# Optimization experiments

Hardware: AMD Instinct MI355X
Metric: run time of the kernel (lower is better)

Reference implementation:

```python
import jax, jax.numpy as jnp
import numpy as np

D_MODEL = 4096
N_TYPES = 6  # fixed event_types list in the module


def setup_inputs() -> dict:
    key = jax.random.key(0)
    ks = jax.random.split(key, 7)
    E, B, d = 131072, 16384, D_MODEL
    return {
        "event_type": jax.random.randint(ks[0], (E,), 0, N_TYPES),
        "confidence": jax.random.uniform(ks[1], (E,), jnp.float32),
        "location": jax.random.uniform(ks[2], (E, 2), jnp.float32) * jnp.array([640.0, 480.0], jnp.float32),
        "batch_idx": jax.random.randint(ks[3], (E,), 0, B),
        "batch_size": B,
        "type_emb": jax.random.normal(ks[4], (N_TYPES, d // 4), jnp.float32),
        "W1": jax.random.normal(ks[5], (d // 2, d // 4 + 3), jnp.float32) / np.sqrt(d // 4 + 3).astype(np.float32),
        "b1": jnp.zeros((d // 2,), jnp.float32),
        "W2": jax.random.normal(ks[6], (d, d // 2), jnp.float32) / np.sqrt(d // 2).astype(np.float32),
        "b2": jnp.zeros((d,), jnp.float32),
    }


def reference(event_type, confidence, location, batch_idx, batch_size, type_emb, W1, b1, W2, b2):
    E = confidence.shape[0]
    B = batch_size
    # per-batch-slot max confidence (empty slots -> -inf)
    seg_max = jax.ops.segment_max(confidence, batch_idx, num_segments=B)
    is_top = confidence == seg_max[batch_idx]
    # first event attaining the max (matches torch's max-over-list semantics)
    cand = jnp.where(is_top, jnp.arange(E), E)
    top_idx = jnp.full((B,), E, dtype=cand.dtype).at[batch_idx].min(cand)
    has_event = top_idx < E
    safe_idx = jnp.where(has_event, top_idx, 0)

    emb = type_emb[event_type[safe_idx]]                 # [B, d/4]
    c = confidence[safe_idx][:, None]                    # [B, 1]
    loc = location[safe_idx] / jnp.array([640.0, 480.0], jnp.float32)  # [B, 2]
    feats = jnp.concatenate([emb, c, loc], axis=-1)      # [B, d/4 + 3]

    h = jax.nn.relu(feats @ W1.T + b1)                   # [B, d/2]
    out = h @ W2.T + b2                                  # [B, d]
    return jnp.where(has_event[:, None], out, jnp.zeros((), out.dtype))
```

## Files before the change

### kernel.cpp

```cpp
#include <hip/hip_runtime.h>
#include <hip/hip_bf16.h>

#define NT 6
#define BM 256
#define BN 256
#define BK 32
#define SLOT 16384

typedef __attribute__((ext_vector_type(4))) float f32x4;
typedef __attribute__((ext_vector_type(8))) short bf16x8;

__device__ __forceinline__ short f2bf(float f) {
    __hip_bfloat16 h = __float2bfloat16(f);
    return (short)__builtin_bit_cast(unsigned short, h);
}

__global__ void k_segmax(const float* __restrict__ conf,
                         const int* __restrict__ bidx,
                         unsigned long long* __restrict__ packed, int E) {
    int i = blockIdx.x * blockDim.x + threadIdx.x;
    if (i >= E) return;
    unsigned cb = __float_as_uint(conf[i]);
    unsigned long long p = ((unsigned long long)cb << 32) | (unsigned)(~(unsigned)i);
    atomicMax(&packed[bidx[i]], p);
}

__global__ void k_base(const float* __restrict__ emb, const float* __restrict__ W1,
                       const float* __restrict__ b1, float* __restrict__ base,
                       float* __restrict__ vecs, int d2, int d4) {
    int gw = (blockIdx.x * blockDim.x + threadIdx.x) >> 6;
    int lane = threadIdx.x & 63;
    int t = gw / d2, n = gw % d2;
    const float* e = emb + (size_t)t * d4;
    const float* w = W1 + (size_t)n * (d4 + 3);
    float s = 0.f;
    for (int k = lane; k < d4; k += 64) s += e[k] * w[k];
#pragma unroll
    for (int m = 32; m; m >>= 1) s += __shfl_xor(s, m);
    if (lane == 0) {
        base[gw] = s + b1[n];
        if (t == 0) {
            vecs[n]          = w[d4];
            vecs[d2 + n]     = w[d4 + 1];
            vecs[2 * d2 + n] = w[d4 + 2];
        }
    }
}

__global__ void k_w2cast(const float* __restrict__ W2, short* __restrict__ W2b, long n) {
    long i = ((long)blockIdx.x * blockDim.x + threadIdx.x) * 8;
    if (i >= n) return;
    bf16x8 v;
#pragma unroll
    for (int j = 0; j < 8; ++j) v[j] = f2bf(W2[i + j]);
    *(bf16x8*)(W2b + i) = v;
}

__global__ void k_h(const unsigned long long* __restrict__ packed,
                    const int* __restrict__ etype, const float* __restrict__ loc,
                    const float* __restrict__ base, const float* __restrict__ vecs,
                    float* __restrict__ mask, short* __restrict__ h, int d2) {
    int b = blockIdx.x;
    int tid = threadIdx.x;
    unsigned long long p = packed[b];
    bool has = (p != 0ULL);
    float conf = 0.f, lx = 0.f, ly = 0.f;
    int t = 0;
    if (has) {
        unsigned idx = ~(unsigned)(p & 0xFFFFFFFFu);
        conf = __uint_as_float((unsigned)(p >> 32));
        t  = etype[idx];
        lx = loc[2 * (size_t)idx]     * (1.0f / 640.0f);
        ly = loc[2 * (size_t)idx + 1] * (1.0f / 480.0f);
    }
    if (tid == 0) mask[b] = has ? 1.0f : 0.0f;
    const float* bs = base + (size_t)t * d2;
    const float* cv = vecs;
    const float* xv = vecs + d2;
    const float* yv = vecs + 2 * d2;
    int n0 = tid * 8;
    bf16x8 v;
#pragma unroll
    for (int j = 0; j < 8; ++j) {
        int n = n0 + j;
        float g = bs[n] + conf * cv[n] + lx * xv[n] + ly * yv[n];
        g = fmaxf(g, 0.f);
        v[j] = has ? f2bf(g) : (short)0;
    }
    *(bf16x8*)(h + (size_t)b * d2 + n0) = v;
}


#define GLL(src, dst) __builtin_amdgcn_global_load_lds(                      \
    (const __attribute__((address_space(1))) void*)(src),                    \
    (__attribute__((address_space(3))) void*)(dst), 16, 0, 0)

#define STAGE4(slotp) do {                                                   \
    GLL(pa0, (slotp) + dA0); GLL(pa1, (slotp) + dA1);                        \
    GLL(pb0, (slotp) + dB0); GLL(pb1, (slotp) + dB1);                        \
    pa0 += BK; pa1 += BK; pb0 += BK; pb1 += BK; } while (0)

#define SB __builtin_amdgcn_sched_barrier(0)

__global__ __launch_bounds__(512, 2)
void k_gemm(const short* __restrict__ A, const short* __restrict__ Bm,
            const float* __restrict__ b2, const float* __restrict__ mask,
            float* __restrict__ C, int M, int N, int K, int nbn) {
    __shared__ __align__(16) short lds[4 * SLOT];

    int tid = threadIdx.x;
    int lane = tid & 63;
    int wave = tid >> 6;
    int wr = wave >> 2, wc = wave & 3;

    int bid = blockIdx.x;
    int wg = (bid & 7) * ((int)gridDim.x >> 3) + (bid >> 3);
    int bm = wg / nbn, bn = wg % nbn;
    int row0 = bm * BM, col0 = bn * BN;

    int srow = tid >> 2;
    int chunkL = (tid & 3) ^ ((srow >> 1) & 3);
    const short* pa0 = A + (size_t)(row0 + srow) * K + chunkL * 8;
    const short* pa1 = pa0 + (size_t)128 * K;
    const short* pb0 = Bm + (size_t)(col0 + srow) * K + chunkL * 8;
    const short* pb1 = pb0 + (size_t)128 * K;
    int dA0 = tid * 8, dA1 = 4096 + tid * 8;
    int dB0 = 8192 + tid * 8, dB1 = 12288 + tid * 8;

    int frow = lane & 15, fk = lane >> 4;
    int cp = fk ^ ((frow >> 1) & 3);
    int aoff = (wr * 128 + frow) * 32 + cp * 8;
    int boff = 8192 + (wc * 64 + frow) * 32 + cp * 8;

    f32x4 acc[8][4] = {};

    int KT = K / BK;

    STAGE4(lds + 0 * SLOT);
    STAGE4(lds + 1 * SLOT);
    STAGE4(lds + 2 * SLOT);
    asm volatile("s_waitcnt vmcnt(8)" ::: "memory");
    __builtin_amdgcn_s_barrier();

#pragma unroll 1
    for (int t = 0; t < KT; ++t) {
        const short* sr = lds + (t & 3) * SLOT;
        bf16x8 afA[4], afB[4], bv[4];
#pragma unroll
        for (int n = 0; n < 4; ++n)
            bv[n] = *(const bf16x8*)(sr + boff + n * 512);
#pragma unroll
        for (int m = 0; m < 4; ++m)
            afA[m] = *(const bf16x8*)(sr + aoff + m * 512);
        SB;
#pragma unroll
        for (int m = 0; m < 4; ++m)
            afB[m] = *(const bf16x8*)(sr + aoff + 2048 + m * 512);
        if (t < KT - 3) {
            short* sw = lds + ((t + 3) & 3) * SLOT;
            STAGE4(sw);
        }
        SB;
        asm volatile("s_waitcnt lgkmcnt(4)" ::: "memory");
        SB;
        __builtin_amdgcn_s_setprio(1);
#pragma unroll
        for (int m = 0; m < 4; ++m)
#pragma unroll
            for (int n = 0; n < 4; ++n)
                acc[m][n] = __builtin_amdgcn_mfma_f32_16x16x32_bf16(
                    afA[m], bv[n], acc[m][n], 0, 0, 0);
        SB;
        asm volatile("s_waitcnt lgkmcnt(0)" ::: "memory");
        SB;
#pragma unroll
        for (int m = 0; m < 4; ++m)
#pragma unroll
            for (int n = 0; n < 4; ++n)
                acc[4 + m][n] = __builtin_amdgcn_mfma_f32_16x16x32_bf16(
                    afB[m], bv[n], acc[4 + m][n], 0, 0, 0);
        __builtin_amdgcn_s_setprio(0);
        if (t < KT - 1) {
            if (t < KT - 3)       asm volatile("s_waitcnt vmcnt(8)" ::: "memory");
            else if (t == KT - 3) asm volatile("s_waitcnt vmcnt(4)" ::: "memory");
            else                  asm volatile("s_waitcnt vmcnt(0)" ::: "memory");
            __builtin_amdgcn_s_barrier();
        }
    }

#pragma unroll
    for (int m = 0; m < 8; ++m) {
        int rbase = row0 + wr * 128 + m * 16 + (lane >> 4) * 4;
#pragma unroll
        for (int j = 0; j < 4; ++j) {
            int r = rbase + j;
            float mk = mask[r];
#pragma unroll
            for (int n = 0; n < 4; ++n) {
                int c = col0 + wc * 64 + n * 16 + frow;
                C[(size_t)r * N + c] = (acc[m][n][j] + b2[c]) * mk;
            }
        }
    }
}

extern "C" void kernel_launch(void* const* d_in, const int* in_sizes, int n_in,
                              void* d_out, int out_size, void* d_ws, size_t ws_size,
                              hipStream_t stream) {
    const int* etype   = (const int*)d_in[0];
    const float* conf  = (const float*)d_in[1];
    const float* loc   = (const float*)d_in[2];
    const int* bidx    = (const int*)d_in[3];
    const float* emb   = (const float*)d_in[5];
    const float* W1    = (const float*)d_in[6];
    const float* b1    = (const float*)d_in[7];
    const float* W2    = (const float*)d_in[8];
    const float* b2    = (const float*)d_in[9];
    float* out = (float*)d_out;

    int E  = in_sizes[0];
    int d2 = in_sizes[7];
    int d  = in_sizes[9];
    int d4 = in_sizes[5] / NT;
    int B  = out_size / d;

    char* ws = (char*)d_ws;
    unsigned long long* packed = (unsigned long long*)ws;
    float* mask = (float*)(ws + (size_t)B * 8);
    float* base = mask + B;
    float* vecs = base + NT * d2;
    short* w2b  = (short*)(vecs + 3 * d2);
    short* h    = w2b + (size_t)d * d2;

    hipMemsetAsync(packed, 0, (size_t)B * 8, stream);
    k_segmax<<<(E + 255) / 256, 256, 0, stream>>>(conf, bidx, packed, E);
    k_base<<<(NT * d2) / 4, 256, 0, stream>>>(emb, W1, b1, base, vecs, d2, d4);
    long nw2 = (long)d * d2;
    k_w2cast<<<(int)(nw2 / 8 / 256), 256, 0, stream>>>(W2, w2b, nw2);
    k_h<<<B, 256, 0, stream>>>(packed, etype, loc, base, vecs, mask, h, d2);
    int nbm = B / BM, nbn = d / BN;
    k_gemm<<<dim3(nbm * nbn), dim3(512), 0, stream>>>(h, w2b, b2, mask, out, B, d, d2, nbn);
}
```

Measured before the change: 312.0 us.

## Software-pipeline LDS fragment loads across K iterations with ping-pong B registers

Restructures the GEMM main loop so the next tile's A(0-3) and B fragments are read from LDS while the second half of the current tile's MFMAs is still issuing, using two B register sets that alternate on a 2x unrolled loop. It also splits the global-to-LDS prefetch so A loads and B loads go out at different points in the iteration, and adds an extra barrier so the slot about to be overwritten has been fully read. The goal is to hide LDS read latency behind MFMA work and smooth out memory traffic. The cost is higher register pressure under the 2-wave occupancy bound, and the loop now assumes KT is even.

```diff
diff --git a/kernel.cpp b/kernel.cpp
--- a/kernel.cpp
+++ b/kernel.cpp
@@ -95,12 +95,46 @@
     (const __attribute__((address_space(1))) void*)(src),                    \
     (__attribute__((address_space(3))) void*)(dst), 16, 0, 0)
 
-#define STAGE4(slotp) do {                                                   \
-    GLL(pa0, (slotp) + dA0); GLL(pa1, (slotp) + dA1);                        \
-    GLL(pb0, (slotp) + dB0); GLL(pb1, (slotp) + dB1);                        \
-    pa0 += BK; pa1 += BK; pb0 += BK; pb1 += BK; } while (0)
-
 #define SB __builtin_amdgcn_sched_barrier(0)
+
+#define BODY(T, CBV, NBV)                                                     \
+  {                                                                           \
+    const short* sr_ = lds + ((T) & 3) * SLOT;                                \
+    short* sw_ = lds + (((T) + 3) & 3) * SLOT;                                \
+    \
+    _Pragma("unroll") for (int m = 0; m < 4; ++m)                             \
+        a47[m] = *(const bf16x8*)(sr_ + aoff + 2048 + m * 512);               \
+    __builtin_amdgcn_s_barrier();                                             \
+    SB;                                                                       \
+    if ((T) < KT - 3) { GLL(pa0, sw_ + dA0); GLL(pa1, sw_ + dA1); }           \
+    __builtin_amdgcn_s_setprio(1);                                            \
+    _Pragma("unroll") for (int m = 0; m < 4; ++m)                             \
+      _Pragma("unroll") for (int n = 0; n < 4; ++n)                           \
+        acc[m][n] = __builtin_amdgcn_mfma_f32_16x16x32_bf16(                  \
+            a03[m], CBV[n], acc[m][n], 0, 0, 0);                              \
+    __builtin_amdgcn_s_setprio(0);                                            \
+                                                                     \
+    if ((T) < KT - 3) { GLL(pb0, sw_ + dB0); GLL(pb1, sw_ + dB1);             \
+                        pa0 += BK; pa1 += BK; pb0 += BK; pb1 += BK; }         \
+    if ((T) < KT - 3)       asm volatile("s_waitcnt vmcnt(8)" ::: "memory");  \
+    else if ((T) == KT - 3) asm volatile("s_waitcnt vmcnt(4)" ::: "memory");  \
+    else if ((T) == KT - 2) asm volatile("s_waitcnt vmcnt(0)" ::: "memory");  \
+    __builtin_amdgcn_s_barrier();                                             \
+    SB;                                                                       \
+    if ((T) < KT - 1) {         \
+      const short* sn_ = lds + (((T) + 1) & 3) * SLOT;                        \
+      _Pragma("unroll") for (int n = 0; n < 4; ++n)                           \
+          NBV[n] = *(const bf16x8*)(sn_ + boff + n * 512);                    \
+      _Pragma("unroll") for (int m = 0; m < 4; ++m)                           \
+          a03[m] = *(const bf16x8*)(sn_ + aoff + m * 512);                    \
+    }                                                                         \
+    __builtin_amdgcn_s_setprio(1);                                            \
+    _Pragma("unroll") for (int m = 0; m < 4; ++m)                             \
+      _Pragma("unroll") for (int n = 0; n < 4; ++n)                           \
+        acc[4 + m][n] = __builtin_amdgcn_mfma_f32_16x16x32_bf16(              \
+            a47[m], CBV[n], acc[4 + m][n], 0, 0, 0);                          \
+    __builtin_amdgcn_s_setprio(0);                                            \
+  }
 
 __global__ __launch_bounds__(512, 2)
 void k_gemm(const short* __restrict__ A, const short* __restrict__ Bm,
@@ -133,59 +167,36 @@
     int boff = 8192 + (wc * 64 + frow) * 32 + cp * 8;
 
     f32x4 acc[8][4] = {};
+    bf16x8 a03[4], a47[4], bv0[4], bv1[4];
 
     int KT = K / BK;
 
-    STAGE4(lds + 0 * SLOT);
-    STAGE4(lds + 1 * SLOT);
-    STAGE4(lds + 2 * SLOT);
+    {
+        short* s0 = lds + 0 * SLOT;
+        GLL(pa0, s0 + dA0); GLL(pa1, s0 + dA1); GLL(pb0, s0 + dB0); GLL(pb1, s0 + dB1);
+        pa0 += BK; pa1 += BK; pb0 += BK; pb1 += BK;
+        short* s1 = lds + 1 * SLOT;
+        GLL(pa0, s1 + dA0); GLL(pa1, s1 + dA1); GLL(pb0, s1 + dB0); GLL(pb1, s1 + dB1);
+        pa0 += BK; pa1 += BK; pb0 += BK; pb1 += BK;
+        short* s2 = lds + 2 * SLOT;
+        GLL(pa0, s2 + dA0); GLL(pa1, s2 + dA1); GLL(pb0, s2 + dB0); GLL(pb1, s2 + dB1);
+        pa0 += BK; pa1 += BK; pb0 += BK; pb1 += BK;
+    }
     asm volatile("s_waitcnt vmcnt(8)" ::: "memory");
     __builtin_amdgcn_s_barrier();
+    SB;
+    {
+        const short* s0 = lds + 0 * SLOT;
+#pragma unroll
+        for (int n = 0; n < 4; ++n) bv0[n] = *(const bf16x8*)(s0 + boff + n * 512);
+#pragma unroll
+        for (int m = 0; m < 4; ++m) a03[m] = *(const bf16x8*)(s0 + aoff + m * 512);
+    }
 
 #pragma unroll 1
-    for (int t = 0; t < KT; ++t) {
-        const short* sr = lds + (t & 3) * SLOT;
-        bf16x8 afA[4], afB[4], bv[4];
-#pragma unroll
-        for (int n = 0; n < 4; ++n)
-            bv[n] = *(const bf16x8*)(sr + boff + n * 512);
-#pragma unroll
-        for (int m = 0; m < 4; ++m)
-            afA[m] = *(const bf16x8*)(sr + aoff + m * 512);
-        SB;
-#pragma unroll
-        for (int m = 0; m < 4; ++m)
-            afB[m] = *(const bf16x8*)(sr + aoff + 2048 + m * 512);
-        if (t < KT - 3) {
-            short* sw = lds + ((t + 3) & 3) * SLOT;
-            STAGE4(sw);
-        }
-        SB;
-        asm volatile("s_waitcnt lgkmcnt(4)" ::: "memory");
-        SB;
-        __builtin_amdgcn_s_setprio(1);
-#pragma unroll
-        for (int m = 0; m < 4; ++m)
-#pragma unroll
-            for (int n = 0; n < 4; ++n)
-                acc[m][n] = __builtin_amdgcn_mfma_f32_16x16x32_bf16(
-                    afA[m], bv[n], acc[m][n], 0, 0, 0);
-        SB;
-        asm volatile("s_waitcnt lgkmcnt(0)" ::: "memory");
-        SB;
-#pragma unroll
-        for (int m = 0; m < 4; ++m)
-#pragma unroll
-            for (int n = 0; n < 4; ++n)
-                acc[4 + m][n] = __builtin_amdgcn_mfma_f32_16x16x32_bf16(
-                    afB[m], bv[n], acc[4 + m][n], 0, 0, 0);
-        __builtin_amdgcn_s_setprio(0);
-        if (t < KT - 1) {
-            if (t < KT - 3)       asm volatile("s_waitcnt vmcnt(8)" ::: "memory");
-            else if (t == KT - 3) asm volatile("s_waitcnt vmcnt(4)" ::: "memory");
-            else                  asm volatile("s_waitcnt vmcnt(0)" ::: "memory");
-            __builtin_amdgcn_s_barrier();
-        }
+    for (int t = 0; t < KT; t += 2) {
+        BODY(t,     bv0, bv1)
+        BODY(t + 1, bv1, bv0)
     }
 
 #pragma unroll
```

Result: no change. 312.5 us (+0.2%).

## Split GEMM K-step into two barrier-synchronized phases interleaving loads and MFMAs

Applied to the files above, without the earlier changes.

Restructures the main GEMM loop into two phases. Each phase issues its LDS fragment reads and half of the global-to-LDS prefetch, then waits at a workgroup barrier before its MFMA block. This is meant to interleave memory traffic with compute across waves in a ping-pong style and spread the global loads out instead of issuing them in one burst. It adds several extra s_barrier calls per iteration and a full lgkmcnt(0) wait, which may stall waves more.

```diff
diff --git a/kernel.cpp b/kernel.cpp
--- a/kernel.cpp
+++ b/kernel.cpp
@@ -95,11 +95,6 @@
     (const __attribute__((address_space(1))) void*)(src),                    \
     (__attribute__((address_space(3))) void*)(dst), 16, 0, 0)
 
-#define STAGE4(slotp) do {                                                   \
-    GLL(pa0, (slotp) + dA0); GLL(pa1, (slotp) + dA1);                        \
-    GLL(pb0, (slotp) + dB0); GLL(pb1, (slotp) + dB1);                        \
-    pa0 += BK; pa1 += BK; pb0 += BK; pb1 += BK; } while (0)
-
 #define SB __builtin_amdgcn_sched_barrier(0)
 
 __global__ __launch_bounds__(512, 2)
@@ -133,35 +128,40 @@
     int boff = 8192 + (wc * 64 + frow) * 32 + cp * 8;
 
     f32x4 acc[8][4] = {};
+    bf16x8 a03[4], a47[4], bv[4];
 
     int KT = K / BK;
 
-    STAGE4(lds + 0 * SLOT);
-    STAGE4(lds + 1 * SLOT);
-    STAGE4(lds + 2 * SLOT);
+    {
+        short* s0 = lds + 0 * SLOT;
+        GLL(pa0, s0 + dA0); GLL(pa1, s0 + dA1); GLL(pb0, s0 + dB0); GLL(pb1, s0 + dB1);
+        pa0 += BK; pa1 += BK; pb0 += BK; pb1 += BK;
+        short* s1 = lds + 1 * SLOT;
+        GLL(pa0, s1 + dA0); GLL(pa1, s1 + dA1); GLL(pb0, s1 + dB0); GLL(pb1, s1 + dB1);
+        pa0 += BK; pa1 += BK; pb0 += BK; pb1 += BK;
+        short* s2 = lds + 2 * SLOT;
+        GLL(pa0, s2 + dA0); GLL(pa1, s2 + dA1); GLL(pb0, s2 + dB0); GLL(pb1, s2 + dB1);
+        pa0 += BK; pa1 += BK; pb0 += BK; pb1 += BK;
+    }
     asm volatile("s_waitcnt vmcnt(8)" ::: "memory");
     __builtin_amdgcn_s_barrier();
 
 #pragma unroll 1
     for (int t = 0; t < KT; ++t) {
         const short* sr = lds + (t & 3) * SLOT;
-        bf16x8 afA[4], afB[4], bv[4];
+        short* sw = lds + ((t + 3) & 3) * SLOT;
+        bool stage = (t < KT - 3);
+
 #pragma unroll
         for (int n = 0; n < 4; ++n)
             bv[n] = *(const bf16x8*)(sr + boff + n * 512);
 #pragma unroll
         for (int m = 0; m < 4; ++m)
-            afA[m] = *(const bf16x8*)(sr + aoff + m * 512);
-        SB;
-#pragma unroll
-        for (int m = 0; m < 4; ++m)
-            afB[m] = *(const bf16x8*)(sr + aoff + 2048 + m * 512);
-        if (t < KT - 3) {
-            short* sw = lds + ((t + 3) & 3) * SLOT;
-            STAGE4(sw);
-        }
-        SB;
-        asm volatile("s_waitcnt lgkmcnt(4)" ::: "memory");
+            a03[m] = *(const bf16x8*)(sr + aoff + m * 512);
+        if (stage) { GLL(pa0, sw + dA0); GLL(pa1, sw + dA1); }
+        SB;
+        __builtin_amdgcn_s_barrier();
+        asm volatile("s_waitcnt lgkmcnt(0)" ::: "memory");
         SB;
         __builtin_amdgcn_s_setprio(1);
 #pragma unroll
@@ -169,17 +169,29 @@
 #pragma unroll
             for (int n = 0; n < 4; ++n)
                 acc[m][n] = __builtin_amdgcn_mfma_f32_16x16x32_bf16(
-                    afA[m], bv[n], acc[m][n], 0, 0, 0);
-        SB;
+                    a03[m], bv[n], acc[m][n], 0, 0, 0);
+        __builtin_amdgcn_s_setprio(0);
+        SB;
+        __builtin_amdgcn_s_barrier();
+
+#pragma unroll
+        for (int m = 0; m < 4; ++m)
+            a47[m] = *(const bf16x8*)(sr + aoff + 2048 + m * 512);
+        if (stage) { GLL(pb0, sw + dB0); GLL(pb1, sw + dB1); }
+        pa0 += BK; pa1 += BK; pb0 += BK; pb1 += BK;
+        SB;
+        __builtin_amdgcn_s_barrier();
         asm volatile("s_waitcnt lgkmcnt(0)" ::: "memory");
         SB;
+        __builtin_amdgcn_s_setprio(1);
 #pragma unroll
         for (int m = 0; m < 4; ++m)
 #pragma unroll
             for (int n = 0; n < 4; ++n)
                 acc[4 + m][n] = __builtin_amdgcn_mfma_f32_16x16x32_bf16(
-                    afB[m], bv[n], acc[4 + m][n], 0, 0, 0);
+                    a47[m], bv[n], acc[4 + m][n], 0, 0, 0);
         __builtin_amdgcn_s_setprio(0);
+        SB;
         if (t < KT - 1) {
             if (t < KT - 3)       asm volatile("s_waitcnt vmcnt(8)" ::: "memory");
             else if (t == KT - 3) asm volatile("s_waitcnt vmcnt(4)" ::: "memory");
```

Result: slower. 326.7 us (+4.7%).
